# Performance work log

Measured on AMD Instinct MI355X. Metric: run time of the kernel, lower is better.

## Reference

```python
import jax, jax.numpy as jnp
import numpy as np

B, N, L, D = 4, 2048, 12, 128  # batch, nodes, in_len, d_model


def _glorot(key, shape):
    fan_in = shape[0]
    return jax.random.normal(key, shape, dtype=jnp.float32) / jnp.sqrt(jnp.float32(fan_in))


def setup_inputs() -> dict:
    key = jax.random.key(0)
    ks = jax.random.split(key, 12)
    x = jax.random.normal(ks[0], (B, N, L, D), dtype=jnp.float32)
    adj = jax.random.uniform(ks[1], (N, N), dtype=jnp.float32)  # dense weighted adjacency
    # mlp2: Linear(L*D -> D)
    W_mlp2 = _glorot(ks[2], (L * D, D)); b_mlp2 = jnp.zeros((D,), jnp.float32)
    # GNN: three DenseSAGEConv layers (lin_rel on aggregated, lin_root on self)
    Wr1 = _glorot(ks[3], (D, D)); Wo1 = _glorot(ks[4], (D, D)); b1 = jnp.zeros((D,), jnp.float32)
    Wr2 = _glorot(ks[5], (D, D)); Wo2 = _glorot(ks[6], (D, D)); b2 = jnp.zeros((D,), jnp.float32)
    Wr3 = _glorot(ks[7], (D, D)); Wo3 = _glorot(ks[8], (D, D)); b3 = jnp.zeros((D,), jnp.float32)
    # mlp1: Linear(D -> L*D)
    W_mlp1 = _glorot(ks[9], (D, L * D)); b_mlp1 = jnp.zeros((L * D,), jnp.float32)
    return {"x": x, "adj": adj, "W_mlp2": W_mlp2, "b_mlp2": b_mlp2,
            "Wr1": Wr1, "Wo1": Wo1, "b1": b1,
            "Wr2": Wr2, "Wo2": Wo2, "b2": b2,
            "Wr3": Wr3, "Wo3": Wo3, "b3": b3,
            "W_mlp1": W_mlp1, "b_mlp1": b_mlp1}


def reference(x, adj, W_mlp2, b_mlp2, Wr1, Wo1, b1, Wr2, Wo2, b2, Wr3, Wo3, b3, W_mlp1, b_mlp1):
    b_, n_, l_, d_ = x.shape
    xf = x.reshape(b_, n_, l_ * d_)                      # 'b n l d -> b n (l d)'
    h = xf @ W_mlp2 + b_mlp2                             # mlp2: (B,N,D)
    deg = jnp.clip(adj.sum(axis=-1, keepdims=True), 1.0, None)  # (N,1)

    def sage(hin, Wr, Wo, bb):
        # mean neighbor aggregation: (adj @ h) / deg, then rel + root linear
        agg = jnp.einsum('mn,bnd->bmd', adj, hin) / deg
        return agg @ Wr + hin @ Wo + bb

    h = jax.nn.relu(sage(h, Wr1, Wo1, b1))
    h = jax.nn.relu(sage(h, Wr2, Wo2, b2))
    h = sage(h, Wr3, Wo3, b3)                            # gnn1_embed output (B,N,D)
    out = h @ W_mlp1 + b_mlp1                            # mlp1: (B,N,L*D)
    return out
```

## Files before the change

### kernel.cpp

```cpp
#include <hip/hip_runtime.h>

typedef __attribute__((ext_vector_type(8))) short short8;
typedef __attribute__((ext_vector_type(4))) float floatx4;

__device__ inline short to_bf16s(float f) {
    unsigned u = __builtin_bit_cast(unsigned, f);
    unsigned r = u + 0x7FFFu + ((u >> 16) & 1u);
    return (short)(r >> 16);
}

__device__ inline void dma16(const short* g, short* l) {
    __builtin_amdgcn_global_load_lds(
        (const __attribute__((address_space(1))) unsigned int*)(const void*)g,
        (__attribute__((address_space(3))) unsigned int*)(void*)l,
        16, 0, 0);
}

template <typename T> struct Ld8;
template <> struct Ld8<short> {
    static __device__ inline short8 load(const short* p) { return *(const short8*)p; }
};
template <> struct Ld8<float> {
    static __device__ inline short8 load(const float* p) {
        float4 f0 = *(const float4*)p;
        float4 f1 = *(const float4*)(p + 4);
        short8 r;
        r[0] = to_bf16s(f0.x); r[1] = to_bf16s(f0.y);
        r[2] = to_bf16s(f0.z); r[3] = to_bf16s(f0.w);
        r[4] = to_bf16s(f1.x); r[5] = to_bf16s(f1.y);
        r[6] = to_bf16s(f1.z); r[7] = to_bf16s(f1.w);
        return r;
    }
};

struct PrepArgs {
    const float* adj;
    const float* W2; const float* W1;
    const float* Wr0; const float* Wo0;
    const float* Wr1; const float* Wo1;
    const float* Wr2; const float* Wo2;
    short* adjS; short* W2T; short* W1T;
    short* BigB0; short* BigB1; short* BigB2;
};

__global__ __launch_bounds__(256) void prep(PrepArgs p) {
    int bid = blockIdx.x;
    if (bid < 2048) {
        const float* src = p.adj + (size_t)bid * 2048;
        float s = 0.f;
        for (int c = threadIdx.x; c < 2048; c += 256) s += src[c];
        __shared__ float red[256];
        red[threadIdx.x] = s;
        __syncthreads();
        for (int st = 128; st > 0; st >>= 1) {
            if (threadIdx.x < st) red[threadIdx.x] += red[threadIdx.x + st];
            __syncthreads();
        }
        float d = red[0];
        d = d < 1.f ? 1.f : d;
        float inv = 1.f / d;
        short* dst = p.adjS + (size_t)bid * 2048;
        for (int c = threadIdx.x; c < 2048; c += 256) dst[c] = to_bf16s(src[c] * inv);
        return;
    }
    int t = bid - 2048;
    __shared__ short tile[32][33];
    int tx = threadIdx.x & 31, ty0 = threadIdx.x >> 5;
    const float* in; int C_; int bx, by;
    short* outp; int outld, copies, copystride, outofs;
    if (t < 192) {
        bx = (t & 3) * 32; by = (t >> 2) * 32; in = p.W2; C_ = 128;
        outp = p.W2T; outld = 1536; copies = 1; copystride = 0; outofs = 0;
    } else if (t < 384) {
        int u = t - 192; bx = (u % 48) * 32; by = (u / 48) * 32; in = p.W1; C_ = 1536;
        outp = p.W1T; outld = 128; copies = 1; copystride = 0; outofs = 0;
    } else {
        int u = t - 384; int l = u / 32; int v = u % 32;
        const float* Wr[3] = {p.Wr0, p.Wr1, p.Wr2};
        const float* Wo[3] = {p.Wo0, p.Wo1, p.Wo2};
        short* BB[3] = {p.BigB0, p.BigB1, p.BigB2};
        outp = BB[l]; outld = 640; C_ = 128;
        if (v < 16) { in = Wr[l]; bx = (v & 3) * 32; by = (v >> 2) * 32;
                      copies = 4; copystride = 128; outofs = 0; }
        else { v -= 16; in = Wo[l]; bx = (v & 3) * 32; by = (v >> 2) * 32;
               copies = 1; copystride = 0; outofs = 512; }
    }
    for (int i = ty0; i < 32; i += 8)
        tile[i][tx] = to_bf16s(in[(size_t)(by + i) * C_ + bx + tx]);
    __syncthreads();
    for (int i = ty0; i < 32; i += 8) {
        short v = tile[tx][i];
        for (int c = 0; c < copies; ++c)
            outp[(size_t)(bx + i) * outld + (by + tx) + outofs + c * copystride] = v;
    }
}

__global__ __launch_bounds__(256) void transposeHp(const short* __restrict__ big,
                                                   short* __restrict__ HT) {
    __shared__ short tile[32][33];
    int bx = blockIdx.x * 32;
    int by = blockIdx.y * 32;
    int b = blockIdx.z;
    int tx = threadIdx.x & 31, ty0 = threadIdx.x >> 5;
    for (int i = ty0; i < 32; i += 8)
        tile[i][tx] = big[(size_t)((by + i) * 4 + b) * 640 + 512 + bx + tx];
    __syncthreads();
    for (int i = ty0; i < 32; i += 8)
        HT[(size_t)(b * 128 + bx + i) * 2048 + by + tx] = tile[tx][i];
}

#define LDSTR 72
#define TILE_ELEMS (64 * LDSTR)

template <typename TA>
__global__ __launch_bounds__(256) void gemm64(
    const TA* __restrict__ A, int lda,
    const short* __restrict__ B, int ldb, int kTiles,
    const float* __restrict__ bias,
    short* __restrict__ C, int ldc, int colofs, int relu, int rowmap) {
    __shared__ __align__(16) short lds[4 * TILE_ELEMS];

    int tid = threadIdx.x;
    int blockM = blockIdx.x * 64;
    int blockN = blockIdx.y * 64;

    int srow = tid >> 3;
    int scol = (tid & 7) * 8;

    const TA* Abase = A + (size_t)blockM * lda;
    const short* Bbase = B + (size_t)blockN * ldb;

    short8 ra0, ra1, rb0, rb1;
    ra0 = Ld8<TA>::load(Abase + (size_t)srow * lda + scol);
    ra1 = Ld8<TA>::load(Abase + (size_t)(srow + 32) * lda + scol);
    rb0 = Ld8<short>::load(Bbase + (size_t)srow * ldb + scol);
    rb1 = Ld8<short>::load(Bbase + (size_t)(srow + 32) * ldb + scol);

    floatx4 acc[2][2];
    #pragma unroll
    for (int i = 0; i < 2; ++i)
        #pragma unroll
        for (int j = 0; j < 2; ++j)
            #pragma unroll
            for (int r = 0; r < 4; ++r) acc[i][j][r] = 0.f;

    int lane = tid & 63;
    int w = tid >> 6;
    int wr = w >> 1, wc = w & 1;
    int quad = lane >> 4, l15 = lane & 15;

    for (int it = 0; it < kTiles; ++it) {
        short* As = lds + (it & 1) * (2 * TILE_ELEMS);
        short* Bs = As + TILE_ELEMS;
        *(short8*)(As + srow * LDSTR + scol) = ra0;
        *(short8*)(As + (srow + 32) * LDSTR + scol) = ra1;
        *(short8*)(Bs + srow * LDSTR + scol) = rb0;
        *(short8*)(Bs + (srow + 32) * LDSTR + scol) = rb1;
        __syncthreads();
        if (it + 1 < kTiles) {
            int ko = (it + 1) * 64;
            ra0 = Ld8<TA>::load(Abase + (size_t)srow * lda + ko + scol);
            ra1 = Ld8<TA>::load(Abase + (size_t)(srow + 32) * lda + ko + scol);
            rb0 = Ld8<short>::load(Bbase + (size_t)srow * ldb + ko + scol);
            rb1 = Ld8<short>::load(Bbase + (size_t)(srow + 32) * ldb + ko + scol);
        }
        const short* Arow = As + (wr * 32 + l15) * LDSTR;
        const short* Brow = Bs + (wc * 32 + l15) * LDSTR;
        #pragma unroll
        for (int ks = 0; ks < 2; ++ks) {
            int kof = ks * 32 + quad * 8;
            short8 a0 = *(const short8*)(Arow + kof);
            short8 a1 = *(const short8*)(Arow + 16 * LDSTR + kof);
            short8 b0 = *(const short8*)(Brow + kof);
            short8 b1 = *(const short8*)(Brow + 16 * LDSTR + kof);
            acc[0][0] = __builtin_amdgcn_mfma_f32_16x16x32_bf16(a0, b0, acc[0][0], 0, 0, 0);
            acc[0][1] = __builtin_amdgcn_mfma_f32_16x16x32_bf16(a0, b1, acc[0][1], 0, 0, 0);
            acc[1][0] = __builtin_amdgcn_mfma_f32_16x16x32_bf16(a1, b0, acc[1][0], 0, 0, 0);
            acc[1][1] = __builtin_amdgcn_mfma_f32_16x16x32_bf16(a1, b1, acc[1][1], 0, 0, 0);
        }
        __syncthreads();
    }

    #pragma unroll
    for (int ti = 0; ti < 2; ++ti) {
        #pragma unroll
        for (int tj = 0; tj < 2; ++tj) {
            int col = blockN + wc * 32 + tj * 16 + l15;
            float bv = bias ? bias[col] : 0.f;
            int row0 = blockM + wr * 32 + ti * 16 + quad * 4;
            #pragma unroll
            for (int r = 0; r < 4; ++r) {
                int m = row0 + r;
                float x = acc[ti][tj][r] + bv;
                if (relu) x = x > 0.f ? x : 0.f;
                int orow = rowmap ? (((m & 2047) << 2) | (m >> 11)) : m;
                C[(size_t)orow * ldc + col + colofs] = to_bf16s(x);
            }
        }
    }
}

template <int MODE>
__global__ __launch_bounds__(256) void gemm128(
    const short* __restrict__ A, int lda,
    const short* __restrict__ B, int ldb,
    int kChunkIters, const float* __restrict__ bias,
    void* __restrict__ Cv, int ldc) {
    __shared__ __align__(16) short As[128 * 64];
    __shared__ __align__(16) short Bs[128 * 64];

    int tid = threadIdx.x;
    int blockM = blockIdx.x * 128;
    int blockN = blockIdx.y * 128;
    int kz = blockIdx.z * kChunkIters * 64;

    const short* Ab = A + (size_t)(blockM + (tid >> 3)) * lda + kz + (tid & 7) * 8;
    const short* Bb = B + (size_t)(blockN + (tid >> 3)) * ldb + kz + (tid & 7) * 8;
    short* Al = As + tid * 8;
    short* Bl = Bs + tid * 8;

    floatx4 acc[4][4];
    #pragma unroll
    for (int i = 0; i < 4; ++i)
        #pragma unroll
        for (int j = 0; j < 4; ++j)
            #pragma unroll
            for (int r = 0; r < 4; ++r) acc[i][j][r] = 0.f;

    int lane = tid & 63;
    int w = tid >> 6;
    int wr = w >> 1, wc = w & 1;
    int quad = lane >> 4, l15 = lane & 15;

    for (int it = 0; it < kChunkIters; ++it) {
        const short* Ag = Ab + it * 64;
        const short* Bg = Bb + it * 64;
        #pragma unroll
        for (int r = 0; r < 4; ++r) {
            dma16(Ag + (size_t)r * 32 * lda, Al + r * 2048);
            dma16(Bg + (size_t)r * 32 * ldb, Bl + r * 2048);
        }
        __syncthreads();
        const short* Ar = As + (wr * 64 + l15) * 64;
        const short* Br = Bs + (wc * 64 + l15) * 64;
        #pragma unroll
        for (int ks = 0; ks < 2; ++ks) {
            int kof = ks * 32 + quad * 8;
            short8 af[4], bfr[4];
            #pragma unroll
            for (int i = 0; i < 4; ++i) af[i] = *(const short8*)(Ar + i * 16 * 64 + kof);
            #pragma unroll
            for (int j = 0; j < 4; ++j) bfr[j] = *(const short8*)(Br + j * 16 * 64 + kof);
            #pragma unroll
            for (int i = 0; i < 4; ++i)
                #pragma unroll
                for (int j = 0; j < 4; ++j)
                    acc[i][j] = __builtin_amdgcn_mfma_f32_16x16x32_bf16(af[i], bfr[j], acc[i][j], 0, 0, 0);
        }
        __syncthreads();
    }

    if (MODE == 1) {
        short* Cb = (short*)Cv;
        int colofs = blockIdx.z * 128;
        #pragma unroll
        for (int ti = 0; ti < 4; ++ti) {
            #pragma unroll
            for (int tj = 0; tj < 4; ++tj) {
                int j = blockN + wc * 64 + tj * 16 + l15;
                int jhi = j >> 7, jlo = j & 127;
                int row0 = blockM + wr * 64 + ti * 16 + quad * 4;
                #pragma unroll
                for (int r = 0; r < 4; ++r) {
                    int m = row0 + r;
                    Cb[(size_t)(m * 4 + jhi) * ldc + jlo + colofs] = to_bf16s(acc[ti][tj][r]);
                }
            }
        }
    } else {
        float* Cf = (float*)Cv;
        #pragma unroll
        for (int ti = 0; ti < 4; ++ti) {
            #pragma unroll
            for (int tj = 0; tj < 4; ++tj) {
                int col = blockN + wc * 64 + tj * 16 + l15;
                float bv = bias[col];
                int row0 = blockM + wr * 64 + ti * 16 + quad * 4;
                #pragma unroll
                for (int r = 0; r < 4; ++r) {
                    int mp = row0 + r;
                    int orow = ((mp & 3) << 11) | (mp >> 2);
                    Cf[(size_t)orow * ldc + col] = acc[ti][tj][r] + bv;
                }
            }
        }
    }
}

extern "C" void kernel_launch(void* const* d_in, const int* in_sizes, int n_in,
                              void* d_out, int out_size, void* d_ws, size_t ws_size,
                              hipStream_t stream) {
    const float* x      = (const float*)d_in[0];
    const float* adj    = (const float*)d_in[1];
    const float* W_mlp2 = (const float*)d_in[2];
    const float* b_mlp2 = (const float*)d_in[3];
    const float* Wr1    = (const float*)d_in[4];
    const float* Wo1    = (const float*)d_in[5];
    const float* b1     = (const float*)d_in[6];
    const float* Wr2    = (const float*)d_in[7];
    const float* Wo2    = (const float*)d_in[8];
    const float* b2     = (const float*)d_in[9];
    const float* Wr3    = (const float*)d_in[10];
    const float* Wo3    = (const float*)d_in[11];
    const float* b3     = (const float*)d_in[12];
    const float* W_mlp1 = (const float*)d_in[13];
    const float* b_mlp1 = (const float*)d_in[14];
    float* out = (float*)d_out;

    char* ws = (char*)d_ws;
    size_t off = 0;
    auto alloc = [&](size_t bytes) -> char* {
        char* p = ws + off;
        off = (off + bytes + 255) & ~(size_t)255;
        return p;
    };
    short* W2T  = (short*)alloc(128 * 1536 * 2);
    short* W1T  = (short*)alloc(1536 * 128 * 2);
    short* BigB[3];
    for (int l = 0; l < 3; ++l) BigB[l] = (short*)alloc(128 * 640 * 2);
    short* adjS = (short*)alloc((size_t)2048 * 2048 * 2);
    short* big[4];
    for (int l = 0; l < 4; ++l) big[l] = (short*)alloc((size_t)8192 * 640 * 2);
    short* HT = (short*)alloc((size_t)512 * 2048 * 2);

    dim3 blk(256);

    PrepArgs pa{adj, W_mlp2, W_mlp1, Wr1, Wo1, Wr2, Wo2, Wr3, Wo3,
                adjS, W2T, W1T, BigB[0], BigB[1], BigB[2]};
    prep<<<2528, blk, 0, stream>>>(pa);

    gemm64<float><<<dim3(128, 2), blk, 0, stream>>>(
        x, 1536, W2T, 1536, 24, b_mlp2, big[0], 640, 512, 0, 1);

    const float* biases[3] = {b1, b2, b3};
    for (int l = 0; l < 3; ++l) {
        transposeHp<<<dim3(4, 64, 4), blk, 0, stream>>>(big[l], HT);
        gemm128<1><<<dim3(16, 4, 4), blk, 0, stream>>>(
            adjS, 2048, HT, 2048, 8, nullptr, big[l], 640);
        gemm64<short><<<dim3(128, 2), blk, 0, stream>>>(
            big[l], 640, BigB[l], 640, 10, biases[l], big[l + 1], 640, 512,
            (l < 2) ? 1 : 0, 0);
    }

    gemm128<2><<<dim3(64, 12, 1), blk, 0, stream>>>(
        big[3] + 512, 640, W1T, 128, 2, b_mlp1, out, 1536);
}
```

Measured before the change: 247.3 us.

## Fuse H transpose into GEMM epilogues and shrink tiles for more blocks

Removes the separate transposeHp kernel by having the mlp2 and SAGE-combine GEMMs write the transposed H copy straight from their epilogues. The small GEMM's M tile is halved to 32 rows, doubling the grid to 512 blocks, and its flags become template parameters. The adjacency GEMM gets its own 64x128 kernel launching 512 blocks, loading tiles with global_load_lds DMA. The cost is scattered, strided HT stores in the non-rowmap epilogue and single-buffered LDS in the new adjacency kernel.

```diff
diff --git a/kernel.cpp b/kernel.cpp
--- a/kernel.cpp
+++ b/kernel.cpp
@@ -1,6 +1,7 @@
 #include <hip/hip_runtime.h>
 
 typedef __attribute__((ext_vector_type(8))) short short8;
+typedef __attribute__((ext_vector_type(4))) short short4v;
 typedef __attribute__((ext_vector_type(4))) float floatx4;
 
 __device__ inline short to_bf16s(float f) {
@@ -95,33 +96,19 @@
     }
 }
 
-__global__ __launch_bounds__(256) void transposeHp(const short* __restrict__ big,
-                                                   short* __restrict__ HT) {
-    __shared__ short tile[32][33];
-    int bx = blockIdx.x * 32;
-    int by = blockIdx.y * 32;
-    int b = blockIdx.z;
-    int tx = threadIdx.x & 31, ty0 = threadIdx.x >> 5;
-    for (int i = ty0; i < 32; i += 8)
-        tile[i][tx] = big[(size_t)((by + i) * 4 + b) * 640 + 512 + bx + tx];
-    __syncthreads();
-    for (int i = ty0; i < 32; i += 8)
-        HT[(size_t)(b * 128 + bx + i) * 2048 + by + tx] = tile[tx][i];
-}
-
 #define LDSTR 72
-#define TILE_ELEMS (64 * LDSTR)
-
-template <typename TA>
-__global__ __launch_bounds__(256) void gemm64(
+
+template <typename TA, int RELU, int ROWMAP, int HTW>
+__global__ __launch_bounds__(256) void gemmT(
     const TA* __restrict__ A, int lda,
     const short* __restrict__ B, int ldb, int kTiles,
     const float* __restrict__ bias,
-    short* __restrict__ C, int ldc, int colofs, int relu, int rowmap) {
-    __shared__ __align__(16) short lds[4 * TILE_ELEMS];
+    short* __restrict__ C, int ldc, int colofs,
+    short* __restrict__ HT) {
+    __shared__ __align__(16) short lds[2 * 96 * LDSTR];
 
     int tid = threadIdx.x;
-    int blockM = blockIdx.x * 64;
+    int blockM = blockIdx.x * 32;
     int blockN = blockIdx.y * 64;
 
     int srow = tid >> 3;
@@ -130,19 +117,16 @@
     const TA* Abase = A + (size_t)blockM * lda;
     const short* Bbase = B + (size_t)blockN * ldb;
 
-    short8 ra0, ra1, rb0, rb1;
-    ra0 = Ld8<TA>::load(Abase + (size_t)srow * lda + scol);
-    ra1 = Ld8<TA>::load(Abase + (size_t)(srow + 32) * lda + scol);
+    short8 ra, rb0, rb1;
+    ra  = Ld8<TA>::load(Abase + (size_t)srow * lda + scol);
     rb0 = Ld8<short>::load(Bbase + (size_t)srow * ldb + scol);
     rb1 = Ld8<short>::load(Bbase + (size_t)(srow + 32) * ldb + scol);
 
-    floatx4 acc[2][2];
+    floatx4 acc[2];
     #pragma unroll
-    for (int i = 0; i < 2; ++i)
-        #pragma unroll
-        for (int j = 0; j < 2; ++j)
-            #pragma unroll
-            for (int r = 0; r < 4; ++r) acc[i][j][r] = 0.f;
+    for (int j = 0; j < 2; ++j)
+        #pragma unroll
+        for (int r = 0; r < 4; ++r) acc[j][r] = 0.f;
 
     int lane = tid & 63;
     int w = tid >> 6;
@@ -150,51 +134,127 @@
     int quad = lane >> 4, l15 = lane & 15;
 
     for (int it = 0; it < kTiles; ++it) {
-        short* As = lds + (it & 1) * (2 * TILE_ELEMS);
-        short* Bs = As + TILE_ELEMS;
-        *(short8*)(As + srow * LDSTR + scol) = ra0;
-        *(short8*)(As + (srow + 32) * LDSTR + scol) = ra1;
+        short* As = lds + (it & 1) * (96 * LDSTR);
+        short* Bs = As + 32 * LDSTR;
+        *(short8*)(As + srow * LDSTR + scol) = ra;
         *(short8*)(Bs + srow * LDSTR + scol) = rb0;
         *(short8*)(Bs + (srow + 32) * LDSTR + scol) = rb1;
         __syncthreads();
         if (it + 1 < kTiles) {
             int ko = (it + 1) * 64;
-            ra0 = Ld8<TA>::load(Abase + (size_t)srow * lda + ko + scol);
-            ra1 = Ld8<TA>::load(Abase + (size_t)(srow + 32) * lda + ko + scol);
+            ra  = Ld8<TA>::load(Abase + (size_t)srow * lda + ko + scol);
             rb0 = Ld8<short>::load(Bbase + (size_t)srow * ldb + ko + scol);
             rb1 = Ld8<short>::load(Bbase + (size_t)(srow + 32) * ldb + ko + scol);
         }
-        const short* Arow = As + (wr * 32 + l15) * LDSTR;
+        const short* Arow = As + (wr * 16 + l15) * LDSTR;
         const short* Brow = Bs + (wc * 32 + l15) * LDSTR;
         #pragma unroll
         for (int ks = 0; ks < 2; ++ks) {
             int kof = ks * 32 + quad * 8;
             short8 a0 = *(const short8*)(Arow + kof);
-            short8 a1 = *(const short8*)(Arow + 16 * LDSTR + kof);
             short8 b0 = *(const short8*)(Brow + kof);
             short8 b1 = *(const short8*)(Brow + 16 * LDSTR + kof);
-            acc[0][0] = __builtin_amdgcn_mfma_f32_16x16x32_bf16(a0, b0, acc[0][0], 0, 0, 0);
-            acc[0][1] = __builtin_amdgcn_mfma_f32_16x16x32_bf16(a0, b1, acc[0][1], 0, 0, 0);
-            acc[1][0] = __builtin_amdgcn_mfma_f32_16x16x32_bf16(a1, b0, acc[1][0], 0, 0, 0);
-            acc[1][1] = __builtin_amdgcn_mfma_f32_16x16x32_bf16(a1, b1, acc[1][1], 0, 0, 0);
-        }
-        __syncthreads();
-    }
-
+            acc[0] = __builtin_amdgcn_mfma_f32_16x16x32_bf16(a0, b0, acc[0], 0, 0, 0);
+            acc[1] = __builtin_amdgcn_mfma_f32_16x16x32_bf16(a0, b1, acc[1], 0, 0, 0);
+        }
+        __syncthreads();
+    }
+
+    #pragma unroll
+    for (int tj = 0; tj < 2; ++tj) {
+        int col = blockN + wc * 32 + tj * 16 + l15;
+        float bv = bias[col];
+        int m0 = blockM + wr * 16 + quad * 4;
+        short4v pk;
+        #pragma unroll
+        for (int r = 0; r < 4; ++r) {
+            int m = m0 + r;
+            float xv = acc[tj][r] + bv;
+            if (RELU) xv = xv > 0.f ? xv : 0.f;
+            short v = to_bf16s(xv);
+            pk[r] = v;
+            int orow = ROWMAP ? (((m & 2047) << 2) | (m >> 11)) : m;
+            C[(size_t)orow * ldc + col + colofs] = v;
+            if (HTW && !ROWMAP) {
+                HT[(size_t)((m & 3) * 128 + col) * 2048 + (m >> 2)] = v;
+            }
+        }
+        if (HTW && ROWMAP) {
+            int b = m0 >> 11, n0 = m0 & 2047;
+            *(short4v*)(HT + (size_t)(b * 128 + col) * 2048 + n0) = pk;
+        }
+    }
+}
+
+__global__ __launch_bounds__(256) void gemmS(const short* __restrict__ A,
+                                             const short* __restrict__ B,
+                                             short* __restrict__ C) {
+    __shared__ __align__(16) short As[64 * 64];
+    __shared__ __align__(16) short Bs[128 * 64];
+
+    int tid = threadIdx.x;
+    int blockM = blockIdx.x * 64;
+    int blockN = blockIdx.y * 128;
+    int kz = blockIdx.z * 512;
+
+    const short* Ab = A + (size_t)(blockM + (tid >> 3)) * 2048 + kz + (tid & 7) * 8;
+    const short* Bb = B + (size_t)(blockN + (tid >> 3)) * 2048 + kz + (tid & 7) * 8;
+    short* Al = As + tid * 8;
+    short* Bl = Bs + tid * 8;
+
+    floatx4 acc[2][4];
+    #pragma unroll
+    for (int i = 0; i < 2; ++i)
+        #pragma unroll
+        for (int j = 0; j < 4; ++j)
+            #pragma unroll
+            for (int r = 0; r < 4; ++r) acc[i][j][r] = 0.f;
+
+    int lane = tid & 63;
+    int w = tid >> 6;
+    int wr = w >> 1, wc = w & 1;
+    int quad = lane >> 4, l15 = lane & 15;
+
+    for (int it = 0; it < 8; ++it) {
+        const short* Ag = Ab + it * 64;
+        const short* Bg = Bb + it * 64;
+        dma16(Ag, Al);
+        dma16(Ag + (size_t)32 * 2048, Al + 2048);
+        #pragma unroll
+        for (int r = 0; r < 4; ++r)
+            dma16(Bg + (size_t)r * 32 * 2048, Bl + r * 2048);
+        __syncthreads();
+        const short* Ar = As + (wr * 32 + l15) * 64;
+        const short* Br = Bs + (wc * 64 + l15) * 64;
+        #pragma unroll
+        for (int ks = 0; ks < 2; ++ks) {
+            int kof = ks * 32 + quad * 8;
+            short8 af[2], bfr[4];
+            #pragma unroll
+            for (int i = 0; i < 2; ++i) af[i] = *(const short8*)(Ar + i * 16 * 64 + kof);
+            #pragma unroll
+            for (int j = 0; j < 4; ++j) bfr[j] = *(const short8*)(Br + j * 16 * 64 + kof);
+            #pragma unroll
+            for (int i = 0; i < 2; ++i)
+                #pragma unroll
+                for (int j = 0; j < 4; ++j)
+                    acc[i][j] = __builtin_amdgcn_mfma_f32_16x16x32_bf16(af[i], bfr[j], acc[i][j], 0, 0, 0);
+        }
+        __syncthreads();
+    }
+
+    int colofs = blockIdx.z * 128;
     #pragma unroll
     for (int ti = 0; ti < 2; ++ti) {
         #pragma unroll
-        for (int tj = 0; tj < 2; ++tj) {
-            int col = blockN + wc * 32 + tj * 16 + l15;
-            float bv = bias ? bias[col] : 0.f;
+        for (int tj = 0; tj < 4; ++tj) {
+            int j = blockN + wc * 64 + tj * 16 + l15;
+            int jhi = j >> 7, jlo = j & 127;
             int row0 = blockM + wr * 32 + ti * 16 + quad * 4;
             #pragma unroll
             for (int r = 0; r < 4; ++r) {
                 int m = row0 + r;
-                float x = acc[ti][tj][r] + bv;
-                if (relu) x = x > 0.f ? x : 0.f;
-                int orow = rowmap ? (((m & 2047) << 2) | (m >> 11)) : m;
-                C[(size_t)orow * ldc + col + colofs] = to_bf16s(x);
+                C[(size_t)(m * 4 + jhi) * 640 + jlo + colofs] = to_bf16s(acc[ti][tj][r]);
             }
         }
     }
@@ -260,24 +320,7 @@
         __syncthreads();
     }
 
-    if (MODE == 1) {
-        short* Cb = (short*)Cv;
-        int colofs = blockIdx.z * 128;
-        #pragma unroll
-        for (int ti = 0; ti < 4; ++ti) {
-            #pragma unroll
-            for (int tj = 0; tj < 4; ++tj) {
-                int j = blockN + wc * 64 + tj * 16 + l15;
-                int jhi = j >> 7, jlo = j & 127;
-                int row0 = blockM + wr * 64 + ti * 16 + quad * 4;
-                #pragma unroll
-                for (int r = 0; r < 4; ++r) {
-                    int m = row0 + r;
-                    Cb[(size_t)(m * 4 + jhi) * ldc + jlo + colofs] = to_bf16s(acc[ti][tj][r]);
-                }
-            }
-        }
-    } else {
+    {
         float* Cf = (float*)Cv;
         #pragma unroll
         for (int ti = 0; ti < 4; ++ti) {
@@ -339,17 +382,20 @@
                 adjS, W2T, W1T, BigB[0], BigB[1], BigB[2]};
     prep<<<2528, blk, 0, stream>>>(pa);
 
-    gemm64<float><<<dim3(128, 2), blk, 0, stream>>>(
-        x, 1536, W2T, 1536, 24, b_mlp2, big[0], 640, 512, 0, 1);
-
-    const float* biases[3] = {b1, b2, b3};
+    gemmT<float, 0, 1, 1><<<dim3(256, 2), blk, 0, stream>>>(
+        x, 1536, W2T, 1536, 24, b_mlp2, big[0], 640, 512, HT);
+
     for (int l = 0; l < 3; ++l) {
-        transposeHp<<<dim3(4, 64, 4), blk, 0, stream>>>(big[l], HT);
-        gemm128<1><<<dim3(16, 4, 4), blk, 0, stream>>>(
-            adjS, 2048, HT, 2048, 8, nullptr, big[l], 640);
-        gemm64<short><<<dim3(128, 2), blk, 0, stream>>>(
-            big[l], 640, BigB[l], 640, 10, biases[l], big[l + 1], 640, 512,
-            (l < 2) ? 1 : 0, 0);
+        gemmS<<<dim3(32, 4, 4), blk, 0, stream>>>(adjS, HT, big[l]);
+        if (l == 0)
+            gemmT<short, 1, 0, 1><<<dim3(256, 2), blk, 0, stream>>>(
+                big[0], 640, BigB[0], 640, 10, b1, big[1], 640, 512, HT);
+        else if (l == 1)
+            gemmT<short, 1, 0, 1><<<dim3(256, 2), blk, 0, stream>>>(
+                big[1], 640, BigB[1], 640, 10, b2, big[2], 640, 512, HT);
+        else
+            gemmT<short, 0, 0, 0><<<dim3(256, 2), blk, 0, stream>>>(
+                big[2], 640, BigB[2], 640, 10, b3, big[3], 640, 512, nullptr);
     }
 
     gemm128<2><<<dim3(64, 12, 1), blk, 0, stream>>>(
```

Measured after the change: 225.6 us. 1.1x faster.
